# Kernel tuning notes

Hardware: AMD Instinct MI355X
Metric: run time of the kernel (lower is better)

## Reference

```python
import jax, jax.numpy as jnp
import numpy as np

BATCH = 32
LATENT = 128
NODE_DIM = 8
MAX_NODES = 512
H_NODE = 128   # node_generator hidden
H_EDGE = 64    # edge_generator hidden


def setup_inputs() -> dict:
    key = jax.random.key(0)
    ks = jax.random.split(key, 9)
    s = 0.02
    return {
        "z":   jax.random.normal(ks[0], (BATCH, LATENT), dtype=jnp.float32),
        "W1":  jax.random.normal(ks[1], (LATENT, H_NODE), dtype=jnp.float32) * s,
        "b1":  jnp.zeros((H_NODE,), dtype=jnp.float32),
        "W2":  jax.random.normal(ks[2], (H_NODE, MAX_NODES * NODE_DIM), dtype=jnp.float32) * s,
        "b2":  jnp.zeros((MAX_NODES * NODE_DIM,), dtype=jnp.float32),
        "E1":  jax.random.normal(ks[3], (2 * NODE_DIM, H_EDGE), dtype=jnp.float32) * s,
        "eb1": jnp.zeros((H_EDGE,), dtype=jnp.float32),
        "E2":  jax.random.normal(ks[4], (H_EDGE, 1), dtype=jnp.float32) * s,
        "eb2": jnp.zeros((1,), dtype=jnp.float32),
    }


def reference(z, W1, b1, W2, b2, E1, eb1, E2, eb2):
    B = z.shape[0]
    # node generator: Linear -> ReLU -> Linear, view to [B, N, node_dim]
    h = jax.nn.relu(z @ W1 + b1)
    nodes = (h @ W2 + b2).reshape(B, MAX_NODES, NODE_DIM)

    # all unordered pairs i < j (static indices)
    iu, ju = np.triu_indices(MAX_NODES, k=1)  # [P]
    pair = jnp.concatenate([nodes[:, iu, :], nodes[:, ju, :]], axis=-1)  # [B, P, 2d]

    # edge generator: Linear -> ReLU -> Linear -> Sigmoid
    he = jax.nn.relu(jnp.einsum("bpd,dh->bph", pair, E1) + eb1)
    p = jax.nn.sigmoid(jnp.einsum("bph,ho->bpo", he, E2) + eb2)[..., 0]  # [B, P]

    adj = jnp.zeros((B, MAX_NODES, MAX_NODES), dtype=p.dtype)
    adj = adj.at[:, iu, ju].set(p).at[:, ju, iu].set(p)
    return nodes, adj
```

## Files before the change

### kernel.cpp

```cpp
#include <hip/hip_runtime.h>

#define BATCH 32
#define LATENT 128
#define NODE_DIM 8
#define MAX_NODES 512
#define H_NODE 128
#define H_EDGE 64

typedef float f32x2 __attribute__((ext_vector_type(2)));

#define UPK_ELEMS (BATCH * 32 * MAX_NODES * 2)

__global__ __launch_bounds__(256) void gen_nodes_uv(
    const float* __restrict__ z,  const float* __restrict__ W1,
    const float* __restrict__ b1, const float* __restrict__ W2,
    const float* __restrict__ b2, const float* __restrict__ E1,
    const float* __restrict__ eb1,
    float* __restrict__ nodes_out, float* __restrict__ UPK,
    float* __restrict__ Vws)
{
    const int b      = blockIdx.x;
    const int mslice = blockIdx.y;
    const int tid    = threadIdx.x;
    const int i0     = mslice * 32;

    __shared__ float sz[LATENT];
    __shared__ float sh[H_NODE];
    __shared__ float sE1[2 * NODE_DIM][H_EDGE];
    __shared__ float sEb1[H_EDGE];
    __shared__ float sN[32][NODE_DIM];

    if (tid < LATENT) sz[tid] = z[b * LATENT + tid];
    for (int idx = tid; idx < 2 * NODE_DIM * H_EDGE; idx += 256)
        (&sE1[0][0])[idx] = E1[idx];
    if (tid < H_EDGE) sEb1[tid] = eb1[tid];
    __syncthreads();

    if (tid < H_NODE) {
        float acc = b1[tid];
#pragma unroll 8
        for (int k = 0; k < LATENT; ++k)
            acc += sz[k] * W1[k * H_NODE + tid];
        sh[tid] = fmaxf(acc, 0.0f);
    }
    __syncthreads();

    const int m = mslice * 256 + tid;
    float acc = b2[m];
#pragma unroll 8
    for (int k = 0; k < H_NODE; ++k)
        acc += sh[k] * W2[(size_t)k * (MAX_NODES * NODE_DIM) + m];
    nodes_out[(size_t)b * (MAX_NODES * NODE_DIM) + m] = acc;
    sN[tid >> 3][tid & 7] = acc;
    __syncthreads();

    {
        const int il = tid & 31;
        const int cg = tid >> 5;
#pragma unroll
        for (int rep = 0; rep < 4; ++rep) {
            const int c2 = rep * 8 + cg;
            const int c  = 2 * c2;
            float ua = sEb1[c], ub = sEb1[c + 1];
#pragma unroll
            for (int d = 0; d < NODE_DIM; ++d) {
                const float nd = sN[il][d];
                ua += nd * sE1[d][c];
                ub += nd * sE1[d][c + 1];
            }
            f32x2 uu = {ua, ub};
            *(f32x2*)&UPK[(((size_t)b * 32 + c2) * MAX_NODES + i0 + il) * 2] = uu;
        }
    }
    {
        const int jl = tid >> 3;
        const int cq = tid & 7;
#pragma unroll
        for (int rep = 0; rep < 4; ++rep) {
            const int c2 = rep * 8 + cq;
            const int c  = 2 * c2;
            float va = 0.f, vb = 0.f;
#pragma unroll
            for (int d = 0; d < NODE_DIM; ++d) {
                const float nd = sN[jl][d];
                va += nd * sE1[NODE_DIM + d][c];
                vb += nd * sE1[NODE_DIM + d][c + 1];
            }
            f32x2 vv = {va, vb};
            *(f32x2*)&Vws[((size_t)(b * MAX_NODES + i0 + jl) << 6) + c] = vv;
        }
    }
}

__global__ __launch_bounds__(256) void edge_gen(
    const float* __restrict__ UPK, const float* __restrict__ Vws,
    const float* __restrict__ E2,  const float* __restrict__ eb2,
    float* __restrict__ adj)
{
    const int b = blockIdx.y;
    int t = blockIdx.x, bi = 0;
    while (t >= 16 - 2 * bi) { t -= 16 - 2 * bi; ++bi; }
    const int jt = 2 * bi + t;
    const bool partial = (jt >> 1) == bi;

    const int tid  = threadIdx.x;
    const int lane = tid & 63;
    const int wv   = tid >> 6;
    const int i0 = bi * 64, j0 = jt * 32;
    const int i  = i0 + lane;

    __shared__ float sV[32][H_EDGE];
    __shared__ float P[32][65];

    {
        const float4* src = (const float4*)(Vws + ((size_t)(b * MAX_NODES + j0) << 6));
        float4* dst = (float4*)&sV[0][0];
        dst[tid]       = src[tid];
        dst[tid + 256] = src[tid + 256];
    }

    f32x2 u[32];
#pragma unroll
    for (int c2 = 0; c2 < 32; ++c2)
        u[c2] = *(const f32x2*)&UPK[(((size_t)b * 32 + c2) * MAX_NODES + i) * 2];

    const float bias = eb2[0];
    const f32x2 zero2 = {0.f, 0.f};
    float* adjb = adj + (size_t)b * MAX_NODES * MAX_NODES;
    __syncthreads();

#pragma unroll 2
    for (int jj = 0; jj < 8; ++jj) {
        const int jl = wv * 8 + jj;
        const int j  = j0 + jl;
        const float* vrow = &sV[jl][0];

        f32x2 a0 = zero2, a1 = zero2;
#pragma unroll
        for (int c2 = 0; c2 < 32; c2 += 2) {
            const f32x2 v0 = *(const f32x2*)(vrow + 2 * c2);
            const f32x2 v1 = *(const f32x2*)(vrow + 2 * c2 + 2);
            const f32x2 w0 = *(const f32x2*)(E2 + 2 * c2);
            const f32x2 w1 = *(const f32x2*)(E2 + 2 * c2 + 2);
            f32x2 t0 = u[c2] + v0;
            f32x2 t1 = u[c2 + 1] + v1;
            t0 = __builtin_elementwise_max(t0, zero2);
            t1 = __builtin_elementwise_max(t1, zero2);
            a0 += w0 * t0;
            a1 += w1 * t1;
        }
        const float x = a0.x + a0.y + a1.x + a1.y + bias;
        const float p = __builtin_amdgcn_rcpf(1.0f + __expf(-x));

        if (!partial) {
            adjb[(size_t)j * MAX_NODES + i] = p;
            P[jl][lane] = p;
        } else {
            if (i <= j) adjb[(size_t)j * MAX_NODES + i] = (i < j) ? p : 0.0f;
            if (i <  j) adjb[(size_t)i * MAX_NODES + j] = p;
        }
    }

    if (!partial) {
        __syncthreads();
        const int mi = i0 + (tid & 63);
        const int q  = tid >> 6;
        float* dst = &adjb[(size_t)mi * MAX_NODES + j0 + q * 8];
        float4 o0, o1;
        o0.x = P[q * 8 + 0][tid & 63]; o0.y = P[q * 8 + 1][tid & 63];
        o0.z = P[q * 8 + 2][tid & 63]; o0.w = P[q * 8 + 3][tid & 63];
        o1.x = P[q * 8 + 4][tid & 63]; o1.y = P[q * 8 + 5][tid & 63];
        o1.z = P[q * 8 + 6][tid & 63]; o1.w = P[q * 8 + 7][tid & 63];
        *(float4*)dst       = o0;
        *(float4*)(dst + 4) = o1;
    }
}

extern "C" void kernel_launch(void* const* d_in, const int* in_sizes, int n_in,
                              void* d_out, int out_size, void* d_ws, size_t ws_size,
                              hipStream_t stream)
{
    const float* z   = (const float*)d_in[0];
    const float* W1  = (const float*)d_in[1];
    const float* b1  = (const float*)d_in[2];
    const float* W2  = (const float*)d_in[3];
    const float* b2  = (const float*)d_in[4];
    const float* E1  = (const float*)d_in[5];
    const float* eb1 = (const float*)d_in[6];
    const float* E2  = (const float*)d_in[7];
    const float* eb2 = (const float*)d_in[8];

    float* nodes_out = (float*)d_out;
    float* adj       = (float*)d_out + BATCH * MAX_NODES * NODE_DIM;

    float* UPK = (float*)d_ws;
    float* Vws = UPK + UPK_ELEMS;

    dim3 g1(BATCH, 16);
    gen_nodes_uv<<<g1, 256, 0, stream>>>(z, W1, b1, W2, b2, E1, eb1,
                                         nodes_out, UPK, Vws);

    dim3 g2(72, BATCH);
    edge_gen<<<g2, 256, 0, stream>>>(UPK, Vws, E2, eb2, adj);
}
```

Baseline: 50.46 us.

## Widen edge tile to 128 rows so each thread handles two i indices

Each edge_gen block now covers 128 i-rows by 32 j-columns, with each thread computing two pairs that share the V row and E2 loads from shared memory. The grid drops from 72 to 40 blocks per batch and the transposed write-back uses a wider P buffer. This reuses V/E2 reads across two outputs and lowers block count, at the cost of double the u registers (64 f32x2 values). That can reduce occupancy and load balance, and the diagonal blocks do more wasted work.

```diff
diff --git a/kernel.cpp b/kernel.cpp
--- a/kernel.cpp
+++ b/kernel.cpp
@@ -99,18 +99,18 @@
 {
     const int b = blockIdx.y;
     int t = blockIdx.x, bi = 0;
-    while (t >= 16 - 2 * bi) { t -= 16 - 2 * bi; ++bi; }
-    const int jt = 2 * bi + t;
-    const bool partial = (jt >> 1) == bi;
+    while (t >= 16 - 4 * bi) { t -= 16 - 4 * bi; ++bi; }
+    const int jt = 4 * bi + t;
+    const bool partial = (jt >> 2) == bi;
 
     const int tid  = threadIdx.x;
     const int lane = tid & 63;
     const int wv   = tid >> 6;
-    const int i0 = bi * 64, j0 = jt * 32;
-    const int i  = i0 + lane;
+    const int i0 = bi * 128, j0 = jt * 32;
+    const int iA = i0 + lane, iB = iA + 64;
 
     __shared__ float sV[32][H_EDGE];
-    __shared__ float P[32][65];
+    __shared__ float P[32][129];
 
     {
         const float4* src = (const float4*)(Vws + ((size_t)(b * MAX_NODES + j0) << 6));
@@ -119,60 +119,71 @@
         dst[tid + 256] = src[tid + 256];
     }
 
-    f32x2 u[32];
-#pragma unroll
-    for (int c2 = 0; c2 < 32; ++c2)
-        u[c2] = *(const f32x2*)&UPK[(((size_t)b * 32 + c2) * MAX_NODES + i) * 2];
-
+    f32x2 uA[32], uB[32];
+#pragma unroll
+    for (int c2 = 0; c2 < 32; ++c2) {
+        const float* base = &UPK[((size_t)b * 32 + c2) * MAX_NODES * 2];
+        uA[c2] = *(const f32x2*)(base + 2 * iA);
+        uB[c2] = *(const f32x2*)(base + 2 * iB);
+    }
+
+    const f32x2* w2 = (const f32x2*)E2;
     const float bias = eb2[0];
-    const f32x2 zero2 = {0.f, 0.f};
+    const f32x2 z2 = {0.f, 0.f};
     float* adjb = adj + (size_t)b * MAX_NODES * MAX_NODES;
     __syncthreads();
 
-#pragma unroll 2
+#pragma unroll 1
     for (int jj = 0; jj < 8; ++jj) {
         const int jl = wv * 8 + jj;
         const int j  = j0 + jl;
-        const float* vrow = &sV[jl][0];
-
-        f32x2 a0 = zero2, a1 = zero2;
-#pragma unroll
-        for (int c2 = 0; c2 < 32; c2 += 2) {
-            const f32x2 v0 = *(const f32x2*)(vrow + 2 * c2);
-            const f32x2 v1 = *(const f32x2*)(vrow + 2 * c2 + 2);
-            const f32x2 w0 = *(const f32x2*)(E2 + 2 * c2);
-            const f32x2 w1 = *(const f32x2*)(E2 + 2 * c2 + 2);
-            f32x2 t0 = u[c2] + v0;
-            f32x2 t1 = u[c2 + 1] + v1;
-            t0 = __builtin_elementwise_max(t0, zero2);
-            t1 = __builtin_elementwise_max(t1, zero2);
-            a0 += w0 * t0;
-            a1 += w1 * t1;
-        }
-        const float x = a0.x + a0.y + a1.x + a1.y + bias;
-        const float p = __builtin_amdgcn_rcpf(1.0f + __expf(-x));
+        const float4* vrow = (const float4*)&sV[jl][0];
+
+        f32x2 aA0 = z2, aA1 = z2, aB0 = z2, aB1 = z2;
+#pragma unroll
+        for (int q = 0; q < 16; ++q) {
+            const float4 vv = vrow[q];
+            const f32x2 v0 = {vv.x, vv.y}, v1 = {vv.z, vv.w};
+            const f32x2 w0 = w2[2 * q], w1 = w2[2 * q + 1];
+            f32x2 s;
+            s = uA[2 * q]     + v0; s = __builtin_elementwise_max(s, z2); aA0 += w0 * s;
+            s = uA[2 * q + 1] + v1; s = __builtin_elementwise_max(s, z2); aA1 += w1 * s;
+            s = uB[2 * q]     + v0; s = __builtin_elementwise_max(s, z2); aB0 += w0 * s;
+            s = uB[2 * q + 1] + v1; s = __builtin_elementwise_max(s, z2); aB1 += w1 * s;
+        }
+        const float xA = aA0.x + aA0.y + aA1.x + aA1.y + bias;
+        const float xB = aB0.x + aB0.y + aB1.x + aB1.y + bias;
+        const float pA = 1.0f / (1.0f + __expf(-xA));
+        const float pB = 1.0f / (1.0f + __expf(-xB));
 
         if (!partial) {
-            adjb[(size_t)j * MAX_NODES + i] = p;
-            P[jl][lane] = p;
+            adjb[(size_t)j * MAX_NODES + iA] = pA;
+            adjb[(size_t)j * MAX_NODES + iB] = pB;
+            P[jl][lane]      = pA;
+            P[jl][64 + lane] = pB;
         } else {
-            if (i <= j) adjb[(size_t)j * MAX_NODES + i] = (i < j) ? p : 0.0f;
-            if (i <  j) adjb[(size_t)i * MAX_NODES + j] = p;
+            if (iA < j)       { adjb[(size_t)j * MAX_NODES + iA] = pA;
+                                adjb[(size_t)iA * MAX_NODES + j] = pA; }
+            else if (iA == j)   adjb[(size_t)j * MAX_NODES + iA] = 0.0f;
+            if (iB < j)       { adjb[(size_t)j * MAX_NODES + iB] = pB;
+                                adjb[(size_t)iB * MAX_NODES + j] = pB; }
+            else if (iB == j)   adjb[(size_t)j * MAX_NODES + iB] = 0.0f;
         }
     }
 
     if (!partial) {
         __syncthreads();
-        const int mi = i0 + (tid & 63);
-        const int q  = tid >> 6;
-        float* dst = &adjb[(size_t)mi * MAX_NODES + j0 + q * 8];
-        float4 o0, o1;
-        o0.x = P[q * 8 + 0][tid & 63]; o0.y = P[q * 8 + 1][tid & 63];
-        o0.z = P[q * 8 + 2][tid & 63]; o0.w = P[q * 8 + 3][tid & 63];
-        o1.x = P[q * 8 + 4][tid & 63]; o1.y = P[q * 8 + 5][tid & 63];
-        o1.z = P[q * 8 + 6][tid & 63]; o1.w = P[q * 8 + 7][tid & 63];
-        *(float4*)dst       = o0;
-        *(float4*)(dst + 4) = o1;
+        const int r = tid & 127;
+        const int h = tid >> 7;
+        const size_t rowbase = (size_t)(i0 + r) * MAX_NODES + j0 + h * 16;
+#pragma unroll
+        for (int g = 0; g < 4; ++g) {
+            const int c0 = h * 16 + 4 * g;
+            float4 o;
+            o.x = P[c0 + 0][r]; o.y = P[c0 + 1][r];
+            o.z = P[c0 + 2][r]; o.w = P[c0 + 3][r];
+            *(float4*)&adjb[rowbase + 4 * g] = o;
+        }
     }
 }
 
@@ -200,6 +211,6 @@
     gen_nodes_uv<<<g1, 256, 0, stream>>>(z, W1, b1, W2, b2, E1, eb1,
                                          nodes_out, UPK, Vws);
 
-    dim3 g2(72, BATCH);
+    dim3 g2(40, BATCH);
     edge_gen<<<g2, 256, 0, stream>>>(UPK, Vws, E2, eb2, adj);
 }
```

After: 59.43 us. 17.8% more time.
